# Kernel tuning notes

Hardware: AMD Instinct MI355X
Metric: run time of the kernel (lower is better)

Reference implementation:

```python
import jax, jax.numpy as jnp
import numpy as np

HEADS = 4
DIM_HEAD = 32


def setup_inputs() -> dict:
    key = jax.random.key(0)
    k1, k2, k3, k4 = jax.random.split(key, 4)
    dim = 128
    hidden = HEADS * DIM_HEAD  # 128
    x = jax.random.normal(k1, (32, dim, 64, 64), dtype=jnp.float32)
    w_qkv = jax.random.normal(k2, (3 * hidden, dim), dtype=jnp.float32) * (1.0 / np.sqrt(dim))
    w_out = jax.random.normal(k3, (dim, hidden), dtype=jnp.float32) * (1.0 / np.sqrt(hidden))
    b_out = jax.random.normal(k4, (dim,), dtype=jnp.float32) * 0.01
    return {"x": x, "w_qkv": w_qkv, "w_out": w_out, "b_out": b_out}


def reference(x, w_qkv, w_out, b_out):
    b, c, h, w = x.shape
    n = h * w
    # 1x1 conv (no bias) == channel matmul
    qkv = jnp.einsum('oc,bchw->bohw', w_qkv, x)  # [b, 3*heads*dh, h, w]
    qkv = qkv.reshape(b, 3, HEADS, DIM_HEAD, n)
    q, k, v = qkv[:, 0], qkv[:, 1], qkv[:, 2]  # each [b, heads, dh, n]
    k = jax.nn.softmax(k, axis=-1)  # softmax over spatial positions
    context = jnp.einsum('bhdn,bhen->bhde', k, v)  # [b, heads, dh, dh]
    out = jnp.einsum('bhde,bhdn->bhen', context, q)  # [b, heads, dh, n]
    out = out.reshape(b, HEADS * DIM_HEAD, h, w)
    # 1x1 conv with bias
    return jnp.einsum('oc,bchw->bohw', w_out, out) + b_out[None, :, None, None]
```

## Files before the change

### kernel.cpp

```cpp
#include <hip/hip_runtime.h>
#include <hip/hip_bf16.h>
#include <math.h>

#define BATCH 32
#define CDIM  128
#define NTOT  4096
#define NCH   16
#define CHN   256
#define TN    64
#define NCH3  16

typedef __attribute__((ext_vector_type(4))) float f32x4;
typedef __attribute__((ext_vector_type(8))) short s16x8;

#define PC_OFF  0
#define PC_SIZE (BATCH * 4 * NCH * 32 * 32)
#define PS_OFF  (PC_OFF + PC_SIZE)
#define PS_SIZE (BATCH * 4 * NCH * 32)
#define MBF_OFF (PS_OFF + PS_SIZE)
#define MBF_SIZE (BATCH * CDIM * CDIM / 2)
#define CTX_OFF (MBF_OFF + MBF_SIZE)
#define CTX_SIZE (BATCH * 4 * 1024)
#define XBT_OFF (CTX_OFF + CTX_SIZE)
#define XBT_SIZE (BATCH * CDIM * NTOT / 2)
#define NEED_BYTES ((size_t)(XBT_OFF + XBT_SIZE) * 4)

static __device__ __forceinline__ unsigned short f2bf(float f) {
    return __builtin_bit_cast(unsigned short, __float2bfloat16(f));
}
static __device__ __forceinline__ unsigned int pack2(float a, float b) {
    return (unsigned int)f2bf(a) | ((unsigned int)f2bf(b) << 16);
}
static __device__ __forceinline__ s16x8 ld_frag_lds(const unsigned int* p, int d0) {
    int4 t;
    t.x = (int)p[d0]; t.y = (int)p[d0 + 1];
    t.z = (int)p[d0 + 2]; t.w = (int)p[d0 + 3];
    return __builtin_bit_cast(s16x8, t);
}

static __device__ __forceinline__ void stage_xT(const float* __restrict__ xc,
                                                unsigned int* __restrict__ xsd,
                                                int tid) {
    const int m  = tid & 15;
    const int cg = tid >> 4;
#pragma unroll
    for (int p = 0; p < 4; ++p) {
        const int c = 2 * cg + 32 * p;
        const f32x4 a0 = *reinterpret_cast<const f32x4*>(xc + (size_t)c * NTOT + 4 * m);
        const f32x4 a1 = *reinterpret_cast<const f32x4*>(xc + (size_t)(c + 1) * NTOT + 4 * m);
#pragma unroll
        for (int jj = 0; jj < 4; ++jj)
            xsd[(4 * m + jj) * 65 + (c >> 1)] = pack2(a0[jj], a1[jj]);
    }
}

template <bool XBT>
__global__ __launch_bounds__(256)
void k1_ctx(const float* __restrict__ x, const float* __restrict__ wqkv,
            float* __restrict__ ws) {
    __shared__ __attribute__((aligned(16))) unsigned short xsT[64 * 130];
    __shared__ __attribute__((aligned(16))) unsigned short ekv[8 * 32 * 68];

    const int j = blockIdx.x, b = blockIdx.y;
    const int tid = threadIdx.x;
    const int l = tid & 63;
    const int w = tid >> 6;
    const int m = l & 15, hq = l >> 4;
    const int mm = tid & 15, cg = tid >> 4;

    s16x8 afr[4][4];
#pragma unroll
    for (int tm = 0; tm < 4; ++tm)
#pragma unroll
        for (int kt = 0; kt < 4; ++kt) {
            const float* wr = wqkv +
                (size_t)(CDIM + 64 * w + 16 * tm + m) * CDIM + 32 * kt + 8 * hq;
            const f32x4 u0 = *reinterpret_cast<const f32x4*>(wr);
            const f32x4 u1 = *reinterpret_cast<const f32x4*>(wr + 4);
            int4 t4;
            t4.x = (int)pack2(u0[0], u0[1]); t4.y = (int)pack2(u0[2], u0[3]);
            t4.z = (int)pack2(u1[0], u1[1]); t4.w = (int)pack2(u1[2], u1[3]);
            afr[tm][kt] = __builtin_bit_cast(s16x8, t4);
        }

    f32x4 cacc[2][2] = {};
    float sacc[4][4] = {};
    const float* xc = x + (size_t)b * CDIM * NTOT + j * CHN;
    unsigned int* xsd = (unsigned int*)xsT;
    unsigned int* ekvd = (unsigned int*)ekv;

    unsigned int xp[16];
    auto load_pack = [&](const float* xptr) {
#pragma unroll
        for (int p = 0; p < 4; ++p) {
            const int c = 2 * cg + 32 * p;
            const f32x4 a0 = *reinterpret_cast<const f32x4*>(xptr + (size_t)c * NTOT + 4 * mm);
            const f32x4 a1 = *reinterpret_cast<const f32x4*>(xptr + (size_t)(c + 1) * NTOT + 4 * mm);
#pragma unroll
            for (int jj = 0; jj < 4; ++jj)
                xp[4 * p + jj] = pack2(a0[jj], a1[jj]);
        }
    };
    auto write_x = [&]() {
#pragma unroll
        for (int p = 0; p < 4; ++p) {
            const int c2 = cg + 16 * p;
#pragma unroll
            for (int jj = 0; jj < 4; ++jj)
                xsd[(4 * mm + jj) * 65 + c2] = xp[4 * p + jj];
        }
    };

    load_pack(xc);

    for (int it = 0; it < CHN / TN; ++it) {
        write_x();
        __syncthreads();
        if (it + 1 < CHN / TN) load_pack(xc + (it + 1) * TN);

        f32x4 acc[4][4] = {};
#pragma unroll
        for (int kt = 0; kt < 4; ++kt) {
#pragma unroll
            for (int tn = 0; tn < 4; ++tn) {
                const s16x8 bfr = ld_frag_lds(xsd, (16 * tn + m) * 65 + 16 * kt + 4 * hq);
#pragma unroll
                for (int tm = 0; tm < 4; ++tm)
                    acc[tm][tn] = __builtin_amdgcn_mfma_f32_16x16x32_bf16(
                        afr[tm][kt], bfr, acc[tm][tn], 0, 0, 0);
            }
        }

        if constexpr (XBT) {
            unsigned int* tb = (unsigned int*)(ws + XBT_OFF) +
                               ((size_t)b * 64 + j * 4 + it) * 4096;
            const int n = tid >> 2, qt = tid & 3;
#pragma unroll
            for (int p = 0; p < 4; ++p) {
                const int cdl = 16 * p + 4 * qt;
                const int src = n * 65 + (cdl ^ ((n & 7) << 2));
                uint4 v;
                v.x = xsd[src]; v.y = xsd[src + 1];
                v.z = xsd[src + 2]; v.w = xsd[src + 3];
                *reinterpret_cast<uint4*>(tb + (size_t)n * 64 + cdl) = v;
            }
        }

        if (w < 2) {
#pragma unroll
            for (int tm = 0; tm < 4; ++tm)
#pragma unroll
                for (int tn = 0; tn < 4; ++tn)
#pragma unroll
                    for (int r = 0; r < 4; ++r) {
                        const int dg = 64 * w + 16 * tm + 4 * hq + r;
                        const float e = __expf(acc[tm][tn][r]);
                        sacc[tm][r] += e;
                        ekv[((dg >> 5) * 32 + (dg & 31)) * 68 + 16 * tn + m] = f2bf(e);
                    }
        } else {
#pragma unroll
            for (int tm = 0; tm < 4; ++tm)
#pragma unroll
                for (int tn = 0; tn < 4; ++tn)
#pragma unroll
                    for (int r = 0; r < 4; ++r) {
                        const int eg = 64 * (w - 2) + 16 * tm + 4 * hq + r;
                        ekv[((4 + (eg >> 5)) * 32 + (eg & 31)) * 68 + 16 * tn + m] =
                            f2bf(acc[tm][tn][r]);
                    }
        }
        __syncthreads();

#pragma unroll
        for (int kt = 0; kt < 2; ++kt) {
            s16x8 va[2], eb[2];
#pragma unroll
            for (int t = 0; t < 2; ++t) {
                va[t] = ld_frag_lds(ekvd,
                    ((4 + w) * 32 + 16 * t + m) * 34 + 16 * kt + 4 * hq);
                eb[t] = ld_frag_lds(ekvd,
                    (w * 32 + 16 * t + m) * 34 + 16 * kt + 4 * hq);
            }
#pragma unroll
            for (int tm = 0; tm < 2; ++tm)
#pragma unroll
                for (int tn = 0; tn < 2; ++tn)
                    cacc[tm][tn] = __builtin_amdgcn_mfma_f32_16x16x32_bf16(
                        va[tm], eb[tn], cacc[tm][tn], 0, 0, 0);
        }
    }

    float* pc = ws + PC_OFF + (size_t)((b * 4 + w) * NCH + j) * 1024;
#pragma unroll
    for (int tm = 0; tm < 2; ++tm)
#pragma unroll
        for (int tn = 0; tn < 2; ++tn)
#pragma unroll
            for (int r = 0; r < 4; ++r)
                pc[(16 * tm + 4 * hq + r) * 32 + 16 * tn + m] = cacc[tm][tn][r];

    if (w < 2) {
#pragma unroll
        for (int tm = 0; tm < 4; ++tm)
#pragma unroll
            for (int r = 0; r < 4; ++r) {
                float s = sacc[tm][r];
                s += __shfl_xor(s, 1);
                s += __shfl_xor(s, 2);
                s += __shfl_xor(s, 4);
                s += __shfl_xor(s, 8);
                if (m == 0) {
                    const int dg = 64 * w + 16 * tm + 4 * hq + r;
                    ws[PS_OFF + (size_t)((b * 4 + (dg >> 5)) * NCH + j) * 32 + (dg & 31)] = s;
                }
            }
    }
}

__global__ __launch_bounds__(256)
void k2a_ctx(float* __restrict__ ws) {
    const int bh = blockIdx.x;
    const int tid = threadIdx.x;
    __shared__ float stotS[32];
    if (tid < 32) {
        float s = 0.f;
        for (int jj = 0; jj < NCH; ++jj)
            s += ws[PS_OFF + (size_t)(bh * NCH + jj) * 32 + tid];
        stotS[tid] = s;
    }
    __syncthreads();
#pragma unroll
    for (int k = 0; k < 4; ++k) {
        const int idx = tid + 256 * k;
        float c = 0.f;
        for (int jj = 0; jj < NCH; ++jj)
            c += ws[PC_OFF + (size_t)(bh * NCH + jj) * 1024 + idx];
        ws[CTX_OFF + (size_t)bh * 1024 + idx] = c / stotS[idx & 31];
    }
}

__global__ __launch_bounds__(256)
void k2b_buildM(const float* __restrict__ wqkv, const float* __restrict__ wout,
                float* __restrict__ ws) {
    const int oq = blockIdx.x;
    const int b  = blockIdx.y;
    const int tid = threadIdx.x;

    __shared__ __attribute__((aligned(16))) float smA[8704];
    __shared__ float G[32][133];
    float* ctxs  = smA;
    float* wouts = smA + 4224;
    unsigned int* wqs = (unsigned int*)smA;

#pragma unroll
    for (int k = 0; k < 16; ++k) {
        const int fid = tid + 256 * k;
        const int h = fid >> 10, rem = fid & 1023;
        const int e = rem >> 5, d = rem & 31;
        ctxs[(h * 32 + d) * 33 + e] = ws[CTX_OFF + (size_t)b * 4096 + fid];
    }
#pragma unroll
    for (int k = 0; k < 16; ++k) {
        const int fid = tid + 256 * k;
        const int o = fid >> 7, c = fid & 127;
        wouts[o * 133 + c] = wout[(size_t)(oq * 32 + o) * CDIM + c];
    }
    __syncthreads();

    {
        const int o2 = tid & 31;
        const int g8 = tid >> 5;
#pragma unroll
        for (int i = 0; i < 16; ++i) {
            const int hd = g8 * 16 + i;
            const int h = hd >> 5;
            float acc = 0.f;
#pragma unroll
            for (int e = 0; e < 32; ++e)
                acc = fmaf(wouts[o2 * 133 + h * 32 + e], ctxs[hd * 33 + e], acc);
            G[o2][hd] = acc;
        }
    }
    __syncthreads();

    {
#pragma unroll
        for (int k = 0; k < 32; ++k) {
            const int fid = tid + 256 * k;
            const int hd = fid >> 6, cd = fid & 63;
            const float2 wv =
                *reinterpret_cast<const float2*>(wqkv + (size_t)hd * CDIM + 2 * cd);
            wqs[hd * 68 + cd] = pack2(wv.x, wv.y);
        }
    }
    __syncthreads();

    {
        const int o3 = tid >> 3;
        const int c0 = tid & 7;
        float Macc[16];
#pragma unroll
        for (int i = 0; i < 16; ++i) Macc[i] = 0.f;
        for (int hd = 0; hd < 128; ++hd) {
            const float gv = G[o3][hd];
            const uint4 w0 = *reinterpret_cast<const uint4*>(&wqs[hd * 68 + c0 * 8]);
            const uint4 w1 = *reinterpret_cast<const uint4*>(&wqs[hd * 68 + c0 * 8 + 4]);
            const unsigned int dw[8] = {w0.x, w0.y, w0.z, w0.w, w1.x, w1.y, w1.z, w1.w};
#pragma unroll
            for (int q = 0; q < 8; ++q) {
                const float lo = __builtin_bit_cast(float, dw[q] << 16);
                const float hi = __builtin_bit_cast(float, dw[q] & 0xffff0000u);
                Macc[2 * q]     = fmaf(gv, lo, Macc[2 * q]);
                Macc[2 * q + 1] = fmaf(gv, hi, Macc[2 * q + 1]);
            }
        }
        unsigned int* mpd = (unsigned int*)((unsigned short*)(ws + MBF_OFF) +
                                            (size_t)b * CDIM * CDIM) +
                            (oq * 32 + o3) * 64 + c0 * 8;
        uint4 s0, s1;
        s0.x = pack2(Macc[0], Macc[1]);   s0.y = pack2(Macc[2], Macc[3]);
        s0.z = pack2(Macc[4], Macc[5]);   s0.w = pack2(Macc[6], Macc[7]);
        s1.x = pack2(Macc[8], Macc[9]);   s1.y = pack2(Macc[10], Macc[11]);
        s1.z = pack2(Macc[12], Macc[13]); s1.w = pack2(Macc[14], Macc[15]);
        *reinterpret_cast<uint4*>(mpd) = s0;
        *reinterpret_cast<uint4*>(mpd + 4) = s1;
    }
}

template <bool XBT>
__global__ __launch_bounds__(256)
void k3_final(const float* __restrict__ x, const float* __restrict__ bout,
              const float* __restrict__ ws, float* __restrict__ out) {
    __shared__ __attribute__((aligned(16))) unsigned int xsd[4160];

    const int j = blockIdx.x, b = blockIdx.y;
    const int tid = threadIdx.x, l = tid & 63, w = tid >> 6;
    const int m = l & 15, hq = l >> 4;

    const unsigned short* mbf =
        (const unsigned short*)(ws + MBF_OFF) + (size_t)b * CDIM * CDIM;
    s16x8 afr[2][4];
#pragma unroll
    for (int tm = 0; tm < 2; ++tm)
#pragma unroll
        for (int kt = 0; kt < 4; ++kt)
            afr[tm][kt] = *reinterpret_cast<const s16x8*>(
                mbf + (size_t)(32 * w + 16 * tm + m) * CDIM + 32 * kt + 8 * hq);
    float bias[2][4];
#pragma unroll
    for (int tm = 0; tm < 2; ++tm)
#pragma unroll
        for (int r = 0; r < 4; ++r)
            bias[tm][r] = bout[32 * w + 16 * tm + 4 * hq + r];

    const float* xc = x + (size_t)b * CDIM * NTOT + j * CHN;
    float* oc = out + (size_t)b * CDIM * NTOT + j * CHN;
    const unsigned int* tb = (const unsigned int*)(ws + XBT_OFF) +
                             ((size_t)b * 64 + j * 4) * 4096;

    for (int it = 0; it < 4; ++it) {
        if constexpr (XBT) {
            const unsigned int* src = tb + it * 4096;
#pragma unroll
            for (int rep = 0; rep < 4; ++rep) {
                const int dw = rep * 1024 + tid * 4;
                *reinterpret_cast<uint4*>(&xsd[dw]) =
                    *reinterpret_cast<const uint4*>(src + dw);
            }
        } else {
            stage_xT(xc + it * TN, xsd, tid);
        }
        __syncthreads();

        f32x4 acc[2][4] = {};
#pragma unroll
        for (int kt = 0; kt < 4; ++kt) {
#pragma unroll
            for (int tn = 0; tn < 4; ++tn) {
                const int nl = 16 * tn + m;
                s16x8 bfr;
                if constexpr (XBT) {
                    const int idx = nl * 64 + ((16 * kt + 4 * hq) ^ ((nl & 7) << 2));
                    bfr = __builtin_bit_cast(
                        s16x8, *reinterpret_cast<const int4*>(&xsd[idx]));
                } else {
                    bfr = ld_frag_lds(xsd, nl * 65 + 16 * kt + 4 * hq);
                }
#pragma unroll
                for (int tm = 0; tm < 2; ++tm)
                    acc[tm][tn] = __builtin_amdgcn_mfma_f32_16x16x32_bf16(
                        afr[tm][kt], bfr, acc[tm][tn], 0, 0, 0);
            }
        }
#pragma unroll
        for (int tm = 0; tm < 2; ++tm)
#pragma unroll
            for (int tn = 0; tn < 4; ++tn)
#pragma unroll
                for (int r = 0; r < 4; ++r)
                    oc[(size_t)(32 * w + 16 * tm + 4 * hq + r) * NTOT +
                       it * TN + 16 * tn + m] = acc[tm][tn][r] + bias[tm][r];
        __syncthreads();
    }
}

extern "C" void kernel_launch(void* const* d_in, const int* in_sizes, int n_in,
                              void* d_out, int out_size, void* d_ws, size_t ws_size,
                              hipStream_t stream) {
    const float* x    = (const float*)d_in[0];
    const float* wqkv = (const float*)d_in[1];
    const float* wout = (const float*)d_in[2];
    const float* bout = (const float*)d_in[3];
    float* out = (float*)d_out;
    float* ws  = (float*)d_ws;

    const bool xbt = ws_size >= NEED_BYTES;

    if (xbt)
        k1_ctx<true><<<dim3(NCH, BATCH), 256, 0, stream>>>(x, wqkv, ws);
    else
        k1_ctx<false><<<dim3(NCH, BATCH), 256, 0, stream>>>(x, wqkv, ws);

    k2a_ctx<<<BATCH * 4, 256, 0, stream>>>(ws);
    k2b_buildM<<<dim3(4, BATCH), 256, 0, stream>>>(wqkv, wout, ws);

    if (xbt)
        k3_final<true><<<dim3(NCH3, BATCH), 256, 0, stream>>>(x, bout, ws, out);
    else
        k3_final<false><<<dim3(NCH3, BATCH), 256, 0, stream>>>(x, bout, ws, out);
}
```

Measured before the change: 87.21 us.

## Halve k1 spatial chunk size to double blocks and drop register prefetch

Doubles the number of spatial chunks in the context kernel (NCH 16→32, CHN 256→128), so twice as many blocks each cover half the positions. The register-based software prefetch of the next x tile is removed in favour of the plain stage_xT helper, and the bf16 transposed-x write offsets and the final kernel's chunk offsets are adjusted to match. The aim is better occupancy and load balance across CUs. The cost is more partial context/sum buffers to reduce and no load/compute overlap inside the loop.

Measured after the change: 117.3 us. 1.34x slower.

```diff
diff --git a/kernel.cpp b/kernel.cpp
--- a/kernel.cpp
+++ b/kernel.cpp
@@ -5,8 +5,8 @@
 #define BATCH 32
 #define CDIM  128
 #define NTOT  4096
-#define NCH   16
-#define CHN   256
+#define NCH   32
+#define CHN   128
 #define TN    64
 #define NCH3  16
 
@@ -66,7 +66,6 @@
     const int l = tid & 63;
     const int w = tid >> 6;
     const int m = l & 15, hq = l >> 4;
-    const int mm = tid & 15, cg = tid >> 4;
 
     s16x8 afr[4][4];
 #pragma unroll
@@ -89,34 +88,9 @@
     unsigned int* xsd = (unsigned int*)xsT;
     unsigned int* ekvd = (unsigned int*)ekv;
 
-    unsigned int xp[16];
-    auto load_pack = [&](const float* xptr) {
-#pragma unroll
-        for (int p = 0; p < 4; ++p) {
-            const int c = 2 * cg + 32 * p;
-            const f32x4 a0 = *reinterpret_cast<const f32x4*>(xptr + (size_t)c * NTOT + 4 * mm);
-            const f32x4 a1 = *reinterpret_cast<const f32x4*>(xptr + (size_t)(c + 1) * NTOT + 4 * mm);
-#pragma unroll
-            for (int jj = 0; jj < 4; ++jj)
-                xp[4 * p + jj] = pack2(a0[jj], a1[jj]);
-        }
-    };
-    auto write_x = [&]() {
-#pragma unroll
-        for (int p = 0; p < 4; ++p) {
-            const int c2 = cg + 16 * p;
-#pragma unroll
-            for (int jj = 0; jj < 4; ++jj)
-                xsd[(4 * mm + jj) * 65 + c2] = xp[4 * p + jj];
-        }
-    };
-
-    load_pack(xc);
-
     for (int it = 0; it < CHN / TN; ++it) {
-        write_x();
+        stage_xT(xc + it * TN, xsd, tid);
         __syncthreads();
-        if (it + 1 < CHN / TN) load_pack(xc + (it + 1) * TN);
 
         f32x4 acc[4][4] = {};
 #pragma unroll
@@ -133,7 +107,7 @@
 
         if constexpr (XBT) {
             unsigned int* tb = (unsigned int*)(ws + XBT_OFF) +
-                               ((size_t)b * 64 + j * 4 + it) * 4096;
+                               ((size_t)b * 64 + j * 2 + it) * 4096;
             const int n = tid >> 2, qt = tid & 3;
 #pragma unroll
             for (int p = 0; p < 4; ++p) {
@@ -354,8 +328,8 @@
         for (int r = 0; r < 4; ++r)
             bias[tm][r] = bout[32 * w + 16 * tm + 4 * hq + r];
 
-    const float* xc = x + (size_t)b * CDIM * NTOT + j * CHN;
-    float* oc = out + (size_t)b * CDIM * NTOT + j * CHN;
+    const float* xc = x + (size_t)b * CDIM * NTOT + j * 256;
+    float* oc = out + (size_t)b * CDIM * NTOT + j * 256;
     const unsigned int* tb = (const unsigned int*)(ws + XBT_OFF) +
                              ((size_t)b * 64 + j * 4) * 4096;
 
```
